# Kernel optimization log

Hardware: AMD Instinct MI355X
Metric: run time of the kernel (lower is better)

## Reference

```python
import jax, jax.numpy as jnp
import numpy as np

LN_EPS = 1e-5


def _forward(x, conv_w, conv_b, ln_w, ln_b, in_proj_w, in_proj_b, out_proj_w, out_proj_b):
    # x: (1, duration, dimensions)
    B, Dur, Dim = x.shape
    xt = jnp.transpose(x, (0, 2, 1))  # (1, Dim, Dur) -> Conv1d NCH layout
    branches = []
    for b in range(Dur):  # structural loop over the 32 conv branches (kernel size k=b+1)
        k = b + 1
        L = Dur - b  # output length duration - k + 1
        w = conv_w[b, :, :, :k]  # (Dim_out, Dim_in, k); padded taps beyond k unused
        y = jax.lax.conv_general_dilated(
            xt, w, window_strides=(1,), padding='VALID',
            dimension_numbers=('NCH', 'OIH', 'NCH'))  # (1, Dim, L)
        y = y + conv_b[b][None, :, None]
        y = jax.nn.gelu(y, approximate=False)  # torch nn.GELU default is exact erf form
        # LayerNorm(normalized_shape=[1, Dim, L]) with batch==1 normalizes the whole tensor
        mu = jnp.mean(y)
        var = jnp.var(y)  # biased, matching torch LayerNorm
        y = (y - mu) * jax.lax.rsqrt(var + LN_EPS)
        y = y * ln_w[b, :, :L][None] + ln_b[b, :, :L][None]
        branches.append(y)  # dropout is identity at inference (p=0.0)
    xc = jnp.concatenate(branches, axis=2)  # (1, Dim, T), T = Dur*(Dur+1)//2
    T = xc.shape[2]

    # nn.MultiheadAttention(embed_dim=T, num_heads=T), batch_first=False: input (L=1, N=Dim, E=T).
    # With seq_len==1, softmax over the single key is exactly 1, so attention output is
    # out_proj(v_proj(value)). value_i = x[:, i, :] broadcast over N, so every batch row of
    # output_i equals out_proj(v_proj(xc[0, i])). Summing over i (the feature loop):
    Wv = in_proj_w[2 * T:]          # (T, T) value slice of in_proj
    bv = in_proj_b[2 * T:]          # (T,)
    V = xc[0] @ Wv.T + bv           # (Dim, T): row i is v-proj of feature i
    S = V.sum(axis=0) @ out_proj_w.T + Dim * out_proj_b  # (T,)  sum over the Dim-term loop
    xa = jnp.broadcast_to(S[None, None, :], (1, Dim, T))  # identical rows, as in torch

    # x.unfold(2, Dur, 4*Dur).mean(-1)
    step = 4 * Dur
    n_w = (T - Dur) // step + 1
    idx = jnp.arange(n_w)[:, None] * step + jnp.arange(Dur)[None, :]  # (n_w, Dur)
    pooled = xa[:, :, idx].mean(-1)  # (1, Dim, n_w)
    return jnp.transpose(pooled, (0, 2, 1))  # (1, n_w, Dim)


def setup_inputs() -> dict:
    key = jax.random.key(0)
    ks = jax.random.split(key, 6)
    Dur, Dim = 32, 256
    T = Dur * (Dur + 1) // 2  # 528
    x = jax.random.normal(ks[0], (1, Dur, Dim), jnp.float32)
    conv_w = jax.random.normal(ks[1], (Dur, Dim, Dim, Dur), jnp.float32) * 0.02  # padded kernel bank
    conv_b = jax.random.normal(ks[2], (Dur, Dim), jnp.float32) * 0.02
    ln_w = jnp.ones((Dur, Dim, Dur), jnp.float32)   # branch b uses [:, :, :Dur-b]
    ln_b = jnp.zeros((Dur, Dim, Dur), jnp.float32)
    in_proj_w = jax.random.normal(ks[3], (3 * T, T), jnp.float32) * 0.02
    in_proj_b = jnp.zeros((3 * T,), jnp.float32)
    out_proj_w = jax.random.normal(ks[4], (T, T), jnp.float32) * 0.02
    out_proj_b = jnp.zeros((T,), jnp.float32)
    return {"x": x, "conv_w": conv_w, "conv_b": conv_b, "ln_w": ln_w, "ln_b": ln_b,
            "in_proj_w": in_proj_w, "in_proj_b": in_proj_b,
            "out_proj_w": out_proj_w, "out_proj_b": out_proj_b}


def reference(x, conv_w, conv_b, ln_w, ln_b, in_proj_w, in_proj_b, out_proj_w, out_proj_b):
    return _forward(x, conv_w, conv_b, ln_w, ln_b, in_proj_w, in_proj_b, out_proj_w, out_proj_b)
```

## Files before the change

### kernel.cpp

```cpp
#include <hip/hip_runtime.h>
#include <math.h>

#define DUR 32
#define DIM 256
#define TT  528

#define WS_BSUM 0
#define WS_BSQ  32
#define WS_CY   64
#define WS_CW   592
#define WS_CB   1120
#define WS_S    1648
#define WS_S2   2176
#define WS_ZERO_FLOATS 1648

__device__ __forceinline__ float gelu_exact(float v) {
    return 0.5f * v * (1.0f + erff(v * 0.70710678118654752f));
}

template<int K4>
__device__ __forceinline__ void conv_body(
    const int bb, const int o0, const int tid,
    const float* __restrict__ x, const float* __restrict__ W,
    const float* __restrict__ convb, const float* __restrict__ lnw,
    const float* __restrict__ lnb, float* __restrict__ ws,
    char* __restrict__ smem, float (* __restrict__ red)[4][32],
    float (* __restrict__ epi)[4][32], float (* __restrict__ sred)[2])
{
    constexpr bool DB  = (K4 < 8);
    constexpr int BUFB = 256 * 16 * K4;
    const int k = bb + 1;
    const int L = 32 - bb;
    const int wave = tid >> 6;
    const int lane = tid & 63;

    float xv[35];
#pragma unroll
    for (int tau = 0; tau < 32; ++tau) xv[tau] = x[tau * DIM + tid];
    xv[32] = 0.f; xv[33] = 0.f; xv[34] = 0.f;

    const float* Wb = W + (size_t)bb * (DIM * DIM * DUR) + (size_t)o0 * (DIM * DUR);

    float4 wreg[K4];
    auto issue = [&](int oo) {
#pragma unroll
        for (int r = 0; r < K4; ++r) {
            const int e = r * 256 + tid;
            wreg[r] = *(const float4*)(Wb + (size_t)oo * (DIM * DUR)
                                        + (e / K4) * 32 + (e % K4) * 4);
        }
    };
    auto stage = [&](int p) {
#pragma unroll
        for (int r = 0; r < K4; ++r) {
            const int e = r * 256 + tid;
            const int n = e / K4, m = e % K4;
            *(float4*)(smem + p * BUFB + (n * K4 + (m + n) % K4) * 16) = wreg[r];
        }
    };

    float cy = 0.f, cw = 0.f, cbv = 0.f, s1 = 0.f, s2 = 0.f;

    auto epilogue = [&](int j) {
        const int o = o0 + j;
        float g = 0.f;
        if (lane < L) {
            const float y = red[j & 1][0][lane] + red[j & 1][1][lane]
                          + red[j & 1][2][lane] + red[j & 1][3][lane]
                          + convb[bb * DIM + o];
            g = gelu_exact(y);
            const float lw = lnw[((size_t)(bb * DIM + o)) * DUR + lane];
            const float lb = lnb[((size_t)(bb * DIM + o)) * DUR + lane];
            cy += g * lw; cw += lw; cbv += lb;
        }
        s1 += g; s2 += g * g;
    };

    issue(0);
#pragma unroll
    for (int oo = 0; oo < 8; ++oo) {
        const int p = DB ? (oo & 1) : 0;
        if (!DB && oo > 0) __syncthreads();
        stage(p);
        __syncthreads();
        if (oo < 7) issue(oo + 1);

        if (oo > 0 && wave == ((oo - 1) & 3)) epilogue(oo - 1);

        float acc[32];
#pragma unroll
        for (int t = 0; t < 32; ++t) acc[t] = 0.f;

        const char* myrow = smem + p * BUFB + tid * (16 * K4);
#pragma unroll
        for (int m = 0; m < K4; ++m) {
            float4 w4 = *(const float4*)(myrow + ((m + tid) % K4) * 16);
            if (4 * m + 0 >= k) w4.x = 0.f;
            if (4 * m + 1 >= k) w4.y = 0.f;
            if (4 * m + 2 >= k) w4.z = 0.f;
            if (4 * m + 3 >= k) w4.w = 0.f;
#pragma unroll
            for (int t = 0; t < 32; ++t) {
                if (t < L) {
                    acc[t] = fmaf(xv[t + 4*m + 0], w4.x, acc[t]);
                    acc[t] = fmaf(xv[t + 4*m + 1], w4.y, acc[t]);
                    acc[t] = fmaf(xv[t + 4*m + 2], w4.z, acc[t]);
                    acc[t] = fmaf(xv[t + 4*m + 3], w4.w, acc[t]);
                }
            }
        }

#pragma unroll
        for (int t = 0; t < 32; ++t) {
            if (t < L) {
                float v = acc[t];
                v += __shfl_down(v, 32, 64);
                v += __shfl_down(v, 16, 64);
                v += __shfl_down(v, 8, 64);
                v += __shfl_down(v, 4, 64);
                v += __shfl_down(v, 2, 64);
                v += __shfl_down(v, 1, 64);
                if (lane == 0) red[oo & 1][wave][t] = v;
            }
        }
    }
    __syncthreads();
    if (wave == 3) epilogue(7);

    if (lane < 32) {
        epi[0][wave][lane] = cy;
        epi[1][wave][lane] = cw;
        epi[2][wave][lane] = cbv;
    }
    {
        float a = s1, b2 = s2;
        a += __shfl_down(a, 32, 64);  b2 += __shfl_down(b2, 32, 64);
        a += __shfl_down(a, 16, 64);  b2 += __shfl_down(b2, 16, 64);
        a += __shfl_down(a, 8, 64);   b2 += __shfl_down(b2, 8, 64);
        a += __shfl_down(a, 4, 64);   b2 += __shfl_down(b2, 4, 64);
        a += __shfl_down(a, 2, 64);   b2 += __shfl_down(b2, 2, 64);
        a += __shfl_down(a, 1, 64);   b2 += __shfl_down(b2, 1, 64);
        if (lane == 0) { sred[wave][0] = a; sred[wave][1] = b2; }
    }
    __syncthreads();
    if (wave == 0 && lane < L) {
        const int tg = bb * 32 - (bb * (bb - 1)) / 2 + lane;
        atomicAdd(ws + WS_CY + tg, epi[0][0][lane] + epi[0][1][lane] + epi[0][2][lane] + epi[0][3][lane]);
        atomicAdd(ws + WS_CW + tg, epi[1][0][lane] + epi[1][1][lane] + epi[1][2][lane] + epi[1][3][lane]);
        atomicAdd(ws + WS_CB + tg, epi[2][0][lane] + epi[2][1][lane] + epi[2][2][lane] + epi[2][3][lane]);
    }
    if (tid == 0) {
        atomicAdd(ws + WS_BSUM + bb, sred[0][0] + sred[1][0] + sred[2][0] + sred[3][0]);
        atomicAdd(ws + WS_BSQ  + bb, sred[0][1] + sred[1][1] + sred[2][1] + sred[3][1]);
    }
}

__global__ __launch_bounds__(256) void conv_kernel(
    const float* __restrict__ x, const float* __restrict__ W,
    const float* __restrict__ convb, const float* __restrict__ lnw,
    const float* __restrict__ lnb, float* ws)
{
    __shared__ char  smem[57344];
    __shared__ float red[2][4][32];
    __shared__ float epi[3][4][32];
    __shared__ float sred[4][2];

    const int bid = blockIdx.x;
    const int bb  = 31 - (bid & 31);
    const int o0  = (bid >> 5) * 8;
    const int tid = threadIdx.x;

    switch (bb >> 2) {
        case 0: conv_body<1>(bb, o0, tid, x, W, convb, lnw, lnb, ws, smem, red, epi, sred); break;
        case 1: conv_body<2>(bb, o0, tid, x, W, convb, lnw, lnb, ws, smem, red, epi, sred); break;
        case 2: conv_body<3>(bb, o0, tid, x, W, convb, lnw, lnb, ws, smem, red, epi, sred); break;
        case 3: conv_body<4>(bb, o0, tid, x, W, convb, lnw, lnb, ws, smem, red, epi, sred); break;
        case 4: conv_body<5>(bb, o0, tid, x, W, convb, lnw, lnb, ws, smem, red, epi, sred); break;
        case 5: conv_body<6>(bb, o0, tid, x, W, convb, lnw, lnb, ws, smem, red, epi, sred); break;
        case 6: conv_body<7>(bb, o0, tid, x, W, convb, lnw, lnb, ws, smem, red, epi, sred); break;
        default: conv_body<8>(bb, o0, tid, x, W, convb, lnw, lnb, ws, smem, red, epi, sred); break;
    }
}

__global__ __launch_bounds__(256) void proj1_kernel(
    float* ws, const float* __restrict__ in_proj_w,
    const float* __restrict__ in_proj_b)
{
    __shared__ float cc[TT];
    __shared__ float mu_s[32], r_s[32];
    __shared__ int map[TT];
    const int n = threadIdx.x;
    if (n < 32) {
        const int Lb = 32 - n;
        const float cnt = 256.f * (float)Lb;
        const float mu = ws[WS_BSUM + n] / cnt;
        const float var = ws[WS_BSQ + n] / cnt - mu * mu;
        mu_s[n] = mu;
        r_s[n] = rsqrtf(var + 1e-5f);
        const int off = n * 32 - (n * (n - 1)) / 2;
        for (int t = 0; t < Lb; ++t) map[off + t] = n;
    }
    __syncthreads();
    for (int t = n; t < TT; t += 256) {
        const int b = map[t];
        cc[t] = (ws[WS_CY + t] - mu_s[b] * ws[WS_CW + t]) * r_s[b] + ws[WS_CB + t];
    }
    __syncthreads();
    const int wave = n >> 6, lane = n & 63;
    const int row = blockIdx.x * 4 + wave;
    const float* Wr = in_proj_w + (size_t)(2 * TT + row) * TT;
    float a = 0.f;
    for (int t = lane; t < TT; t += 64) a = fmaf(Wr[t], cc[t], a);
    a += __shfl_down(a, 32, 64);
    a += __shfl_down(a, 16, 64);
    a += __shfl_down(a, 8, 64);
    a += __shfl_down(a, 4, 64);
    a += __shfl_down(a, 2, 64);
    a += __shfl_down(a, 1, 64);
    if (lane == 0) ws[WS_S + row] = a + 256.f * in_proj_b[2 * TT + row];
}

__global__ __launch_bounds__(256) void proj2a_kernel(
    float* ws, const float* __restrict__ out_proj_w,
    const float* __restrict__ out_proj_b)
{
    const int i = blockIdx.x;
    const int u = (i >> 5) * 128 + (i & 31);
    const int n = threadIdx.x;
    const int wave = n >> 6, lane = n & 63;
    const float* Or = out_proj_w + (size_t)u * TT;
    float a = 0.f;
    for (int t = n; t < TT; t += 256) a = fmaf(Or[t], ws[WS_S + t], a);
    a += __shfl_down(a, 32, 64);
    a += __shfl_down(a, 16, 64);
    a += __shfl_down(a, 8, 64);
    a += __shfl_down(a, 4, 64);
    a += __shfl_down(a, 2, 64);
    a += __shfl_down(a, 1, 64);
    __shared__ float r4[4];
    if (lane == 0) r4[wave] = a;
    __syncthreads();
    if (n == 0) ws[WS_S2 + i] = r4[0] + r4[1] + r4[2] + r4[3] + 256.f * out_proj_b[u];
}

__global__ __launch_bounds__(256) void proj2b_kernel(
    const float* __restrict__ ws, float* __restrict__ out)
{
    const int n = threadIdx.x;
    __shared__ float mv;
    if (n < 64) {
        float v = (n < 32) ? ws[WS_S2 + blockIdx.x * 32 + n] : 0.f;
        v += __shfl_down(v, 16, 64);
        v += __shfl_down(v, 8, 64);
        v += __shfl_down(v, 4, 64);
        v += __shfl_down(v, 2, 64);
        v += __shfl_down(v, 1, 64);
        if (n == 0) mv = v * (1.0f / 32.0f);
    }
    __syncthreads();
    out[blockIdx.x * 256 + n] = mv;
}

extern "C" void kernel_launch(void* const* d_in, const int* in_sizes, int n_in,
                              void* d_out, int out_size, void* d_ws, size_t ws_size,
                              hipStream_t stream)
{
    const float* x   = (const float*)d_in[0];
    const float* W   = (const float*)d_in[1];
    const float* cb  = (const float*)d_in[2];
    const float* lnw = (const float*)d_in[3];
    const float* lnb = (const float*)d_in[4];
    const float* ipw = (const float*)d_in[5];
    const float* ipb = (const float*)d_in[6];
    const float* opw = (const float*)d_in[7];
    const float* opb = (const float*)d_in[8];
    float* ws  = (float*)d_ws;
    float* out = (float*)d_out;

    hipMemsetAsync(ws, 0, WS_ZERO_FLOATS * sizeof(float), stream);
    conv_kernel<<<1024, 256, 0, stream>>>(x, W, cb, lnw, lnb, ws);
    proj1_kernel<<<132, 256, 0, stream>>>(ws, ipw, ipb);
    proj2a_kernel<<<128, 256, 0, stream>>>(ws, opw, opb);
    proj2b_kernel<<<4, 256, 0, stream>>>(ws, out);
}
```

Baseline: 444.8 us.

## Restructure conv as one wave per (branch, output channel) without LDS staging

The conv kernel now assigns one wavefront to each (branch, output channel) pair. Each wave reads its weight taps straight from global memory into registers, with per-branch template specialisation so no work is wasted on padded taps or outputs. The shared-memory staging, double buffering and block-wide syncs are removed. The LayerNorm weight and bias column sums move into a separate prep kernel, and the two out-projection kernels are merged into one. The cost is more atomics per output (one wave per channel), much less in-block reuse of x, and an extra kernel launch.

Result: slower. 476.2 us (+7.1%).

```diff
diff --git a/kernel.cpp b/kernel.cpp
--- a/kernel.cpp
+++ b/kernel.cpp
@@ -11,174 +11,155 @@
 #define WS_CW   592
 #define WS_CB   1120
 #define WS_S    1648
-#define WS_S2   2176
-#define WS_ZERO_FLOATS 1648
+#define WS_ZERO_FLOATS 592
 
 __device__ __forceinline__ float gelu_exact(float v) {
     return 0.5f * v * (1.0f + erff(v * 0.70710678118654752f));
 }
 
-template<int K4>
-__device__ __forceinline__ void conv_body(
-    const int bb, const int o0, const int tid,
+__device__ __forceinline__ float wave_reduce_down(float v) {
+    v += __shfl_down(v, 32, 64);
+    v += __shfl_down(v, 16, 64);
+    v += __shfl_down(v, 8, 64);
+    v += __shfl_down(v, 4, 64);
+    v += __shfl_down(v, 2, 64);
+    v += __shfl_down(v, 1, 64);
+    return v;
+}
+
+__global__ __launch_bounds__(256) void prep_kernel(
+    const float* __restrict__ lnw, const float* __restrict__ lnb,
+    float* __restrict__ ws)
+{
+    const int bid = blockIdx.x;
+    const int n = threadIdx.x;
+    int b = 0, off = 0;
+    while (bid >= off + (DUR - b)) { off += DUR - b; ++b; }
+    const int t = bid - off;
+    const float lw = lnw[((size_t)(b * DIM + n)) * DUR + t];
+    const float lb = lnb[((size_t)(b * DIM + n)) * DUR + t];
+    __shared__ float rw[4], rb[4];
+    const int wave = n >> 6, lane = n & 63;
+    const float a = wave_reduce_down(lw);
+    const float c = wave_reduce_down(lb);
+    if (lane == 0) { rw[wave] = a; rb[wave] = c; }
+    __syncthreads();
+    if (n == 0) {
+        ws[WS_CW + bid] = rw[0] + rw[1] + rw[2] + rw[3];
+        ws[WS_CB + bid] = rb[0] + rb[1] + rb[2] + rb[3];
+    }
+}
+
+template<int BB>
+__device__ __forceinline__ void wave_body(
+    const int o, const int lane,
     const float* __restrict__ x, const float* __restrict__ W,
     const float* __restrict__ convb, const float* __restrict__ lnw,
-    const float* __restrict__ lnb, float* __restrict__ ws,
-    char* __restrict__ smem, float (* __restrict__ red)[4][32],
-    float (* __restrict__ epi)[4][32], float (* __restrict__ sred)[2])
-{
-    constexpr bool DB  = (K4 < 8);
-    constexpr int BUFB = 256 * 16 * K4;
-    const int k = bb + 1;
-    const int L = 32 - bb;
-    const int wave = tid >> 6;
-    const int lane = tid & 63;
-
-    float xv[35];
-#pragma unroll
-    for (int tau = 0; tau < 32; ++tau) xv[tau] = x[tau * DIM + tid];
-    xv[32] = 0.f; xv[33] = 0.f; xv[34] = 0.f;
-
-    const float* Wb = W + (size_t)bb * (DIM * DIM * DUR) + (size_t)o0 * (DIM * DUR);
-
-    float4 wreg[K4];
-    auto issue = [&](int oo) {
-#pragma unroll
-        for (int r = 0; r < K4; ++r) {
-            const int e = r * 256 + tid;
-            wreg[r] = *(const float4*)(Wb + (size_t)oo * (DIM * DUR)
-                                        + (e / K4) * 32 + (e % K4) * 4);
-        }
-    };
-    auto stage = [&](int p) {
-#pragma unroll
-        for (int r = 0; r < K4; ++r) {
-            const int e = r * 256 + tid;
-            const int n = e / K4, m = e % K4;
-            *(float4*)(smem + p * BUFB + (n * K4 + (m + n) % K4) * 16) = wreg[r];
-        }
-    };
-
-    float cy = 0.f, cw = 0.f, cbv = 0.f, s1 = 0.f, s2 = 0.f;
-
-    auto epilogue = [&](int j) {
-        const int o = o0 + j;
-        float g = 0.f;
-        if (lane < L) {
-            const float y = red[j & 1][0][lane] + red[j & 1][1][lane]
-                          + red[j & 1][2][lane] + red[j & 1][3][lane]
-                          + convb[bb * DIM + o];
-            g = gelu_exact(y);
-            const float lw = lnw[((size_t)(bb * DIM + o)) * DUR + lane];
-            const float lb = lnb[((size_t)(bb * DIM + o)) * DUR + lane];
-            cy += g * lw; cw += lw; cbv += lb;
-        }
-        s1 += g; s2 += g * g;
-    };
-
-    issue(0);
-#pragma unroll
-    for (int oo = 0; oo < 8; ++oo) {
-        const int p = DB ? (oo & 1) : 0;
-        if (!DB && oo > 0) __syncthreads();
-        stage(p);
-        __syncthreads();
-        if (oo < 7) issue(oo + 1);
-
-        if (oo > 0 && wave == ((oo - 1) & 3)) epilogue(oo - 1);
-
-        float acc[32];
-#pragma unroll
-        for (int t = 0; t < 32; ++t) acc[t] = 0.f;
-
-        const char* myrow = smem + p * BUFB + tid * (16 * K4);
-#pragma unroll
-        for (int m = 0; m < K4; ++m) {
-            float4 w4 = *(const float4*)(myrow + ((m + tid) % K4) * 16);
-            if (4 * m + 0 >= k) w4.x = 0.f;
-            if (4 * m + 1 >= k) w4.y = 0.f;
-            if (4 * m + 2 >= k) w4.z = 0.f;
-            if (4 * m + 3 >= k) w4.w = 0.f;
-#pragma unroll
-            for (int t = 0; t < 32; ++t) {
-                if (t < L) {
-                    acc[t] = fmaf(xv[t + 4*m + 0], w4.x, acc[t]);
-                    acc[t] = fmaf(xv[t + 4*m + 1], w4.y, acc[t]);
-                    acc[t] = fmaf(xv[t + 4*m + 2], w4.z, acc[t]);
-                    acc[t] = fmaf(xv[t + 4*m + 3], w4.w, acc[t]);
-                }
+    float* __restrict__ ws)
+{
+    constexpr int k  = BB + 1;
+    constexpr int L  = DUR - BB;
+    constexpr int K4 = (k + 3) / 4;
+
+    const float* Wo = W + (size_t)(BB * DIM + o) * (DIM * DUR);
+
+    float acc[L];
+#pragma unroll
+    for (int t = 0; t < L; ++t) acc[t] = 0.f;
+
+#pragma unroll 1
+    for (int c = 0; c < 4; ++c) {
+        const int i = c * 64 + lane;
+        float4 w4[K4];
+        const float* Wl = Wo + i * DUR;
+#pragma unroll
+        for (int m = 0; m < K4; ++m) w4[m] = *(const float4*)(Wl + 4 * m);
+        float xv[32];
+#pragma unroll
+        for (int tau = 0; tau < 32; ++tau) xv[tau] = x[tau * DIM + i];
+#pragma unroll
+        for (int t = 0; t < L; ++t) {
+#pragma unroll
+            for (int m = 0; m < K4; ++m) {
+                acc[t] = fmaf(xv[t + 4*m + 0], w4[m].x, acc[t]);
+                if (4*m + 1 < k) acc[t] = fmaf(xv[t + 4*m + 1], w4[m].y, acc[t]);
+                if (4*m + 2 < k) acc[t] = fmaf(xv[t + 4*m + 2], w4[m].z, acc[t]);
+                if (4*m + 3 < k) acc[t] = fmaf(xv[t + 4*m + 3], w4[m].w, acc[t]);
             }
         }
-
-#pragma unroll
-        for (int t = 0; t < 32; ++t) {
-            if (t < L) {
-                float v = acc[t];
-                v += __shfl_down(v, 32, 64);
-                v += __shfl_down(v, 16, 64);
-                v += __shfl_down(v, 8, 64);
-                v += __shfl_down(v, 4, 64);
-                v += __shfl_down(v, 2, 64);
-                v += __shfl_down(v, 1, 64);
-                if (lane == 0) red[oo & 1][wave][t] = v;
-            }
-        }
-    }
-    __syncthreads();
-    if (wave == 3) epilogue(7);
-
-    if (lane < 32) {
-        epi[0][wave][lane] = cy;
-        epi[1][wave][lane] = cw;
-        epi[2][wave][lane] = cbv;
-    }
-    {
-        float a = s1, b2 = s2;
-        a += __shfl_down(a, 32, 64);  b2 += __shfl_down(b2, 32, 64);
-        a += __shfl_down(a, 16, 64);  b2 += __shfl_down(b2, 16, 64);
-        a += __shfl_down(a, 8, 64);   b2 += __shfl_down(b2, 8, 64);
-        a += __shfl_down(a, 4, 64);   b2 += __shfl_down(b2, 4, 64);
-        a += __shfl_down(a, 2, 64);   b2 += __shfl_down(b2, 2, 64);
-        a += __shfl_down(a, 1, 64);   b2 += __shfl_down(b2, 1, 64);
-        if (lane == 0) { sred[wave][0] = a; sred[wave][1] = b2; }
-    }
-    __syncthreads();
-    if (wave == 0 && lane < L) {
-        const int tg = bb * 32 - (bb * (bb - 1)) / 2 + lane;
-        atomicAdd(ws + WS_CY + tg, epi[0][0][lane] + epi[0][1][lane] + epi[0][2][lane] + epi[0][3][lane]);
-        atomicAdd(ws + WS_CW + tg, epi[1][0][lane] + epi[1][1][lane] + epi[1][2][lane] + epi[1][3][lane]);
-        atomicAdd(ws + WS_CB + tg, epi[2][0][lane] + epi[2][1][lane] + epi[2][2][lane] + epi[2][3][lane]);
-    }
-    if (tid == 0) {
-        atomicAdd(ws + WS_BSUM + bb, sred[0][0] + sred[1][0] + sred[2][0] + sred[3][0]);
-        atomicAdd(ws + WS_BSQ  + bb, sred[0][1] + sred[1][1] + sred[2][1] + sred[3][1]);
-    }
-}
-
-__global__ __launch_bounds__(256) void conv_kernel(
+    }
+
+    float mine = 0.f;
+#pragma unroll
+    for (int t = 0; t < L; ++t) {
+        float v = acc[t];
+        v += __shfl_xor(v, 1, 64);
+        v += __shfl_xor(v, 2, 64);
+        v += __shfl_xor(v, 4, 64);
+        v += __shfl_xor(v, 8, 64);
+        v += __shfl_xor(v, 16, 64);
+        v += __shfl_xor(v, 32, 64);
+        if (lane == t) mine = v;
+    }
+
+    constexpr int tg = BB * DUR - (BB * (BB - 1)) / 2;
+    float g = 0.f;
+    if (lane < L) {
+        const float y = mine + convb[BB * DIM + o];
+        g = gelu_exact(y);
+        const float lw = lnw[((size_t)(BB * DIM + o)) * DUR + lane];
+        atomicAdd(ws + WS_CY + tg + lane, g * lw);
+    }
+    const float s1 = wave_reduce_down(g);
+    const float s2 = wave_reduce_down(g * g);
+    if (lane == 0) {
+        atomicAdd(ws + WS_BSUM + BB, s1);
+        atomicAdd(ws + WS_BSQ  + BB, s2);
+    }
+}
+
+__global__ __launch_bounds__(256, 4) void conv_kernel(
     const float* __restrict__ x, const float* __restrict__ W,
     const float* __restrict__ convb, const float* __restrict__ lnw,
-    const float* __restrict__ lnb, float* ws)
-{
-    __shared__ char  smem[57344];
-    __shared__ float red[2][4][32];
-    __shared__ float epi[3][4][32];
-    __shared__ float sred[4][2];
-
-    const int bid = blockIdx.x;
-    const int bb  = 31 - (bid & 31);
-    const int o0  = (bid >> 5) * 8;
-    const int tid = threadIdx.x;
-
-    switch (bb >> 2) {
-        case 0: conv_body<1>(bb, o0, tid, x, W, convb, lnw, lnb, ws, smem, red, epi, sred); break;
-        case 1: conv_body<2>(bb, o0, tid, x, W, convb, lnw, lnb, ws, smem, red, epi, sred); break;
-        case 2: conv_body<3>(bb, o0, tid, x, W, convb, lnw, lnb, ws, smem, red, epi, sred); break;
-        case 3: conv_body<4>(bb, o0, tid, x, W, convb, lnw, lnb, ws, smem, red, epi, sred); break;
-        case 4: conv_body<5>(bb, o0, tid, x, W, convb, lnw, lnb, ws, smem, red, epi, sred); break;
-        case 5: conv_body<6>(bb, o0, tid, x, W, convb, lnw, lnb, ws, smem, red, epi, sred); break;
-        case 6: conv_body<7>(bb, o0, tid, x, W, convb, lnw, lnb, ws, smem, red, epi, sred); break;
-        default: conv_body<8>(bb, o0, tid, x, W, convb, lnw, lnb, ws, smem, red, epi, sred); break;
+    float* __restrict__ ws)
+{
+    const int q    = blockIdx.x * 4 + (threadIdx.x >> 6);
+    const int lane = threadIdx.x & 63;
+    const int bb   = 31 - (q & 31);
+    const int o    = q >> 5;
+    switch (bb) {
+        case  0: wave_body< 0>(o, lane, x, W, convb, lnw, ws); break;
+        case  1: wave_body< 1>(o, lane, x, W, convb, lnw, ws); break;
+        case  2: wave_body< 2>(o, lane, x, W, convb, lnw, ws); break;
+        case  3: wave_body< 3>(o, lane, x, W, convb, lnw, ws); break;
+        case  4: wave_body< 4>(o, lane, x, W, convb, lnw, ws); break;
+        case  5: wave_body< 5>(o, lane, x, W, convb, lnw, ws); break;
+        case  6: wave_body< 6>(o, lane, x, W, convb, lnw, ws); break;
+        case  7: wave_body< 7>(o, lane, x, W, convb, lnw, ws); break;
+        case  8: wave_body< 8>(o, lane, x, W, convb, lnw, ws); break;
+        case  9: wave_body< 9>(o, lane, x, W, convb, lnw, ws); break;
+        case 10: wave_body<10>(o, lane, x, W, convb, lnw, ws); break;
+        case 11: wave_body<11>(o, lane, x, W, convb, lnw, ws); break;
+        case 12: wave_body<12>(o, lane, x, W, convb, lnw, ws); break;
+        case 13: wave_body<13>(o, lane, x, W, convb, lnw, ws); break;
+        case 14: wave_body<14>(o, lane, x, W, convb, lnw, ws); break;
+        case 15: wave_body<15>(o, lane, x, W, convb, lnw, ws); break;
+        case 16: wave_body<16>(o, lane, x, W, convb, lnw, ws); break;
+        case 17: wave_body<17>(o, lane, x, W, convb, lnw, ws); break;
+        case 18: wave_body<18>(o, lane, x, W, convb, lnw, ws); break;
+        case 19: wave_body<19>(o, lane, x, W, convb, lnw, ws); break;
+        case 20: wave_body<20>(o, lane, x, W, convb, lnw, ws); break;
+        case 21: wave_body<21>(o, lane, x, W, convb, lnw, ws); break;
+        case 22: wave_body<22>(o, lane, x, W, convb, lnw, ws); break;
+        case 23: wave_body<23>(o, lane, x, W, convb, lnw, ws); break;
+        case 24: wave_body<24>(o, lane, x, W, convb, lnw, ws); break;
+        case 25: wave_body<25>(o, lane, x, W, convb, lnw, ws); break;
+        case 26: wave_body<26>(o, lane, x, W, convb, lnw, ws); break;
+        case 27: wave_body<27>(o, lane, x, W, convb, lnw, ws); break;
+        case 28: wave_body<28>(o, lane, x, W, convb, lnw, ws); break;
+        case 29: wave_body<29>(o, lane, x, W, convb, lnw, ws); break;
+        case 30: wave_body<30>(o, lane, x, W, convb, lnw, ws); break;
+        default: wave_body<31>(o, lane, x, W, convb, lnw, ws); break;
     }
 }
 
@@ -211,45 +192,30 @@
     const float* Wr = in_proj_w + (size_t)(2 * TT + row) * TT;
     float a = 0.f;
     for (int t = lane; t < TT; t += 64) a = fmaf(Wr[t], cc[t], a);
-    a += __shfl_down(a, 32, 64);
-    a += __shfl_down(a, 16, 64);
-    a += __shfl_down(a, 8, 64);
-    a += __shfl_down(a, 4, 64);
-    a += __shfl_down(a, 2, 64);
-    a += __shfl_down(a, 1, 64);
+    a = wave_reduce_down(a);
     if (lane == 0) ws[WS_S + row] = a + 256.f * in_proj_b[2 * TT + row];
 }
 
-__global__ __launch_bounds__(256) void proj2a_kernel(
-    float* ws, const float* __restrict__ out_proj_w,
-    const float* __restrict__ out_proj_b)
-{
-    const int i = blockIdx.x;
-    const int u = (i >> 5) * 128 + (i & 31);
-    const int n = threadIdx.x;
+__global__ __launch_bounds__(256) void proj2_kernel(
+    const float* __restrict__ ws, const float* __restrict__ out_proj_w,
+    const float* __restrict__ out_proj_b, float* __restrict__ out)
+{
+    const int w = blockIdx.x, n = threadIdx.x;
     const int wave = n >> 6, lane = n & 63;
-    const float* Or = out_proj_w + (size_t)u * TT;
-    float a = 0.f;
-    for (int t = n; t < TT; t += 256) a = fmaf(Or[t], ws[WS_S + t], a);
-    a += __shfl_down(a, 32, 64);
-    a += __shfl_down(a, 16, 64);
-    a += __shfl_down(a, 8, 64);
-    a += __shfl_down(a, 4, 64);
-    a += __shfl_down(a, 2, 64);
-    a += __shfl_down(a, 1, 64);
-    __shared__ float r4[4];
-    if (lane == 0) r4[wave] = a;
-    __syncthreads();
-    if (n == 0) ws[WS_S2 + i] = r4[0] + r4[1] + r4[2] + r4[3] + 256.f * out_proj_b[u];
-}
-
-__global__ __launch_bounds__(256) void proj2b_kernel(
-    const float* __restrict__ ws, float* __restrict__ out)
-{
-    const int n = threadIdx.x;
+    __shared__ float s2s[32];
     __shared__ float mv;
+    for (int jj = 0; jj < 8; ++jj) {
+        const int j = wave * 8 + jj;
+        const int u = w * 128 + j;
+        const float* Or = out_proj_w + (size_t)u * TT;
+        float a = 0.f;
+        for (int t = lane; t < TT; t += 64) a = fmaf(Or[t], ws[WS_S + t], a);
+        a = wave_reduce_down(a);
+        if (lane == 0) s2s[j] = a + 256.f * out_proj_b[u];
+    }
+    __syncthreads();
     if (n < 64) {
-        float v = (n < 32) ? ws[WS_S2 + blockIdx.x * 32 + n] : 0.f;
+        float v = (n < 32) ? s2s[n] : 0.f;
         v += __shfl_down(v, 16, 64);
         v += __shfl_down(v, 8, 64);
         v += __shfl_down(v, 4, 64);
@@ -258,7 +224,7 @@
         if (n == 0) mv = v * (1.0f / 32.0f);
     }
     __syncthreads();
-    out[blockIdx.x * 256 + n] = mv;
+    out[w * 256 + n] = mv;
 }
 
 extern "C" void kernel_launch(void* const* d_in, const int* in_sizes, int n_in,
@@ -278,8 +244,8 @@
     float* out = (float*)d_out;
 
     hipMemsetAsync(ws, 0, WS_ZERO_FLOATS * sizeof(float), stream);
-    conv_kernel<<<1024, 256, 0, stream>>>(x, W, cb, lnw, lnb, ws);
+    prep_kernel<<<TT, 256, 0, stream>>>(lnw, lnb, ws);
+    conv_kernel<<<2048, 256, 0, stream>>>(x, W, cb, lnw, ws);
     proj1_kernel<<<132, 256, 0, stream>>>(ws, ipw, ipb);
-    proj2a_kernel<<<128, 256, 0, stream>>>(ws, opw, opb);
-    proj2b_kernel<<<4, 256, 0, stream>>>(ws, out);
-}
+    proj2_kernel<<<4, 256, 0, stream>>>(ws, opw, opb, out);
+}
```
